# Kernel tuning notes

Measured on AMD Instinct MI355X. Metric: run time of the kernel, lower is better.

Reference implementation:

```python
import jax, jax.numpy as jnp
import numpy as np

N_FFT = 2048
HOP = 512


def _hann(n):
    # scipy.signal.get_window('hann', n, fftbins=True)
    return (0.5 - 0.5 * np.cos(2.0 * np.pi * np.arange(n) / n)).astype(np.float32)


def setup_inputs() -> dict:
    key = jax.random.key(0)
    k1, k2 = jax.random.split(key)
    B, T, F = 8, 1000, N_FFT // 2 + 1
    real_stft = jax.random.normal(k1, (B, 1, T, F), dtype=jnp.float32)
    imag_stft = jax.random.normal(k2, (B, 1, T, F), dtype=jnp.float32)

    # Windowed IDFT matrices, exactly as ISTFT.__init__ builds conv weights.
    n = N_FFT
    x, y = np.meshgrid(np.arange(n), np.arange(n))
    ang = 2.0 * np.pi * ((x * y) % n) / n  # angle of omega**(x*y), omega = exp(2*pi*i/n)
    win = _hann(n)  # win_length == n_fft -> pad_center is a no-op
    W_real = (np.cos(ang) / n * win[:, None]).astype(np.float32)
    W_imag = (np.sin(ang) / n * win[:, None]).astype(np.float32)

    return {
        "real_stft": real_stft,
        "imag_stft": imag_stft,
        "W_real": jnp.asarray(W_real),
        "W_imag": jnp.asarray(W_imag),
        "window": jnp.asarray(win),
        "length": 511488,  # HOP * (n_frames - 1) with n_frames = 1000
    }


def reference(real_stft, imag_stft, W_real, W_imag, window, length):
    n_fft, hop = N_FFT, HOP
    B = real_stft.shape[0]

    fr = jnp.swapaxes(real_stft[:, 0], 1, 2)  # (B, n_fft//2+1, T)
    fi = jnp.swapaxes(imag_stft[:, 0], 1, 2)
    # Hermitian symmetry -> full (B, n_fft, T) spectrum
    full_r = jnp.concatenate([fr, jnp.flip(fr[:, 1:-1, :], axis=1)], axis=1)
    full_i = jnp.concatenate([fi, -jnp.flip(fi[:, 1:-1, :], axis=1)], axis=1)

    # center=True and length given (static Python int)
    padded_length = length + n_fft
    n_frames = min(fr.shape[2], -(-padded_length // hop))

    # windowed real IFFT per frame: s[b, o, t]
    s = (jnp.einsum('oi,bit->bot', W_real, full_r[:, :, :n_frames])
         - jnp.einsum('oi,bit->bot', W_imag, full_i[:, :, :n_frames]))

    L = n_fft + hop * (n_frames - 1)
    # fused overlap-add via scatter-add
    idx = (jnp.arange(n_frames)[:, None] * hop + jnp.arange(n_fft)[None, :]).reshape(-1)
    frames = jnp.swapaxes(s, 1, 2).reshape(B, -1)  # (B, n_frames*n_fft)
    y = jnp.zeros((B, L), s.dtype).at[:, idx].add(frames)

    # window sum-square normalization (librosa.filters.window_sumsquare)
    wss = jnp.zeros((L,), window.dtype).at[idx].add(jnp.tile(window ** 2, n_frames))
    tiny = jnp.finfo(window.dtype).tiny
    nz = wss > tiny
    y = jnp.where(nz[None, :], y / jnp.where(nz, wss, 1.0)[None, :], y)

    start = n_fft // 2
    return y[:, start:start + length]
```

## Files before the change

### kernel.cpp

```cpp
#include <hip/hip_runtime.h>


#define N_FFT    2048
#define HOP      512
#define T_FRAMES 1000
#define F_BINS   1025
#define OUT_LEN  511488
#define FPB      8
#define BPB      125
#define OAF      5632

#define P(a) ((a) + ((a) >> 4))

__device__ __forceinline__ void cmul(float ar, float ai, float br, float bi,
                                     float& cr, float& ci) {
    cr = ar * br - ai * bi;
    ci = ar * bi + ai * br;
}

__global__ __launch_bounds__(256) void istft_oa_kernel(const float* __restrict__ re,
                                                       const float* __restrict__ im,
                                                       const float* __restrict__ win,
                                                       float* __restrict__ scratch,
                                                       float* __restrict__ out) {
    __shared__ __align__(16) float2 buf[1088];
    __shared__ __align__(16) float2 oa2[OAF / 2];

    const int j   = blockIdx.x;
    const int b   = blockIdx.y;
    const int tid = threadIdx.x;
    const int t0  = j * FPB;

    {
        float4* z4 = (float4*)oa2;
        #pragma unroll
        for (int e = 0; e < 6; ++e) {
            int idx = tid + 256 * e;
            if (idx < 1408) z4[idx] = make_float4(0.f, 0.f, 0.f, 0.f);
        }
    }

    const float Sc = 0.5f / 1024.f;
    const float2* w2v = (const float2*)win;

    for (int d = 0; d < FPB; ++d) {
        const int f = b * T_FRAMES + t0 + d;
        const float* fr = re + (size_t)f * F_BINS;
        const float* fi = im + (size_t)f * F_BINS;

        #pragma unroll
        for (int k0 = 0; k0 < 1024; k0 += 256) {
            int k = k0 + tid;
            float ar = fr[k];
            float ai = (k == 0) ? 0.f : fi[k];
            int mk = 1024 - k;
            float br = fr[mk];
            float bi = (mk == 1024) ? 0.f : fi[mk];
            float dr = ar - br, di = ai + bi;
            float ang = 3.14159265358979f * (float)k / 1024.f;
            float sn, cs;
            __sincosf(ang, &sn, &cs);
            float Zr = (ar + br - (cs * di + sn * dr)) * Sc;
            float Zi = (ai - bi + (cs * dr - sn * di)) * Sc;
            unsigned r10 = __brev((unsigned)k) >> 22;
            int rk = (int)(((r10 & 0x155u) << 1) | ((r10 >> 1) & 0x155u));
            buf[P(rk)] = make_float2(Zr, Zi);
        }
        __syncthreads();

        {
            int base = tid << 2;
            int i0 = P(base), i1 = P(base + 1), i2 = P(base + 2), i3 = P(base + 3);
            float2 a = buf[i0], bb = buf[i1], c = buf[i2], dd = buf[i3];
            float t0r = a.x + c.x,  t0i = a.y + c.y;
            float t1r = a.x - c.x,  t1i = a.y - c.y;
            float t2r = bb.x + dd.x, t2i = bb.y + dd.y;
            float t3r = bb.x - dd.x, t3i = bb.y - dd.y;
            buf[i0] = make_float2(t0r + t2r, t0i + t2i);
            buf[i1] = make_float2(t1r - t3i, t1i + t3r);
            buf[i2] = make_float2(t0r - t2r, t0i - t2i);
            buf[i3] = make_float2(t1r + t3i, t1i - t3r);
        }

        #pragma unroll
        for (int s = 1; s < 4; ++s) {
            __builtin_amdgcn_wave_barrier();
            const int hm = 1 << (2 * s);
            const int jj   = tid & (hm - 1);
            const int base = ((tid - jj) << 2) + jj;
            float ang = 1.57079632679f * (float)jj / (float)hm;
            float s1, c1;
            __sincosf(ang, &s1, &c1);
            float c2, s2, c3, s3;
            cmul(c1, s1, c1, s1, c2, s2);
            cmul(c2, s2, c1, s1, c3, s3);

            int i0 = P(base), i1 = P(base + hm), i2 = P(base + 2 * hm), i3 = P(base + 3 * hm);
            float2 a = buf[i0], bb = buf[i1], c = buf[i2], dd = buf[i3];
            float br_, bi_, cr_, ci_, dr_, di_;
            cmul(bb.x, bb.y, c1, s1, br_, bi_);
            cmul(c.x,  c.y,  c2, s2, cr_, ci_);
            cmul(dd.x, dd.y, c3, s3, dr_, di_);

            float t0r = a.x + cr_, t0i = a.y + ci_;
            float t1r = a.x - cr_, t1i = a.y - ci_;
            float t2r = br_ + dr_, t2i = bi_ + di_;
            float t3r = br_ - dr_, t3i = bi_ - di_;
            buf[i0] = make_float2(t0r + t2r, t0i + t2i);
            buf[i1] = make_float2(t1r - t3i, t1i + t3r);
            buf[i2] = make_float2(t0r - t2r, t0i - t2i);
            buf[i3] = make_float2(t1r + t3i, t1i - t3r);
        }
        __syncthreads();

        {
            float ang = 1.57079632679f * (float)tid / 256.f;
            float s1, c1;
            __sincosf(ang, &s1, &c1);
            float c2, s2, c3, s3;
            cmul(c1, s1, c1, s1, c2, s2);
            cmul(c2, s2, c1, s1, c3, s3);

            int i0 = P(tid), i1 = P(tid + 256), i2 = P(tid + 512), i3 = P(tid + 768);
            float2 a = buf[i0], bb = buf[i1], c = buf[i2], dd = buf[i3];
            float br_, bi_, cr_, ci_, dr_, di_;
            cmul(bb.x, bb.y, c1, s1, br_, bi_);
            cmul(c.x,  c.y,  c2, s2, cr_, ci_);
            cmul(dd.x, dd.y, c3, s3, dr_, di_);

            float t0r = a.x + cr_, t0i = a.y + ci_;
            float t1r = a.x - cr_, t1i = a.y - ci_;
            float t2r = br_ + dr_, t2i = bi_ + di_;
            float t3r = br_ - dr_, t3i = bi_ - di_;

            float2 z0 = make_float2(t0r + t2r, t0i + t2i);
            float2 z1 = make_float2(t1r - t3i, t1i + t3r);
            float2 z2 = make_float2(t0r - t2r, t0i - t2i);
            float2 z3 = make_float2(t1r + t3i, t1i - t3r);

            float2 w0 = w2v[tid],       w1 = w2v[tid + 256];
            float2 w2 = w2v[tid + 512], w3 = w2v[tid + 768];

            const int base2 = 256 * d;
            float2 v;
            v = oa2[base2 + tid];
            v.x += z0.x * w0.x;  v.y += z0.y * w0.y;
            oa2[base2 + tid] = v;
            v = oa2[base2 + tid + 256];
            v.x += z1.x * w1.x;  v.y += z1.y * w1.y;
            oa2[base2 + tid + 256] = v;
            v = oa2[base2 + tid + 512];
            v.x += z2.x * w2.x;  v.y += z2.y * w2.y;
            oa2[base2 + tid + 512] = v;
            v = oa2[base2 + tid + 768];
            v.x += z3.x * w3.x;  v.y += z3.y * w3.y;
            oa2[base2 + tid + 768] = v;
        }
        __syncthreads();
    }

    const float inv = 2.f / 3.f;
    const float4* oa4 = (const float4*)oa2;
    float4* o4 = (float4*)(out + (size_t)b * OUT_LEN + (size_t)4096 * j + 512);
    #pragma unroll
    for (int e = 0; e < 3; ++e) {
        int idx = tid + 256 * e;
        if (idx < 640) {
            float4 v = oa4[384 + idx];
            o4[idx] = make_float4(v.x * inv, v.y * inv, v.z * inv, v.w * inv);
        }
    }
    float4* sc4 = (float4*)(scratch + (((size_t)b * BPB + j) * 2) * 1536);
    #pragma unroll
    for (int e = 0; e < 3; ++e) {
        int idx = tid + 256 * e;
        float4 v = (idx < 384) ? oa4[idx] : oa4[640 + idx];
        sc4[idx] = v;
    }
}

__global__ __launch_bounds__(256) void seam_kernel(const float* __restrict__ scratch,
                                                   const float* __restrict__ win,
                                                   float* __restrict__ out) {
    const int g = blockIdx.x;
    const int b = blockIdx.y;

    #pragma unroll
    for (int e = 0; e < 6; ++e) {
        int i = threadIdx.x + 256 * e;
        int n = 4096 * g + i;
        int m = n - 1024;
        if (m < 0 || m >= OUT_LEN) continue;
        float s = 0.f;
        if (g > 0)
            s += scratch[(((size_t)b * BPB + (g - 1)) * 2 + 1) * 1536 + i];
        if (g < BPB)
            s += scratch[(((size_t)b * BPB + g) * 2) * 1536 + i];
        float r;
        if (n >= 1536 && n < 512000) {
            r = s * (2.f / 3.f);
        } else {
            int thi = n >> 9; if (thi > T_FRAMES - 1) thi = T_FRAMES - 1;
            int tlo = (n - (N_FFT - HOP)) >> 9; if (tlo < 0) tlo = 0;
            float wss = 0.f;
            for (int t = tlo; t <= thi; ++t) {
                float w = win[n - (t << 9)];
                wss += w * w;
            }
            r = (wss > 1.17549435e-38f) ? s / wss : s;
        }
        out[(size_t)b * OUT_LEN + m] = r;
    }
}

extern "C" void kernel_launch(void* const* d_in, const int* in_sizes, int n_in,
                              void* d_out, int out_size, void* d_ws, size_t ws_size,
                              hipStream_t stream) {
    const float* re  = (const float*)d_in[0];
    const float* im  = (const float*)d_in[1];
    const float* win = (const float*)d_in[4];
    float* out = (float*)d_out;

    float* scratch = (float*)d_ws;

    istft_oa_kernel<<<dim3(BPB, 8), 256, 0, stream>>>(re, im, win, scratch, out);
    seam_kernel<<<dim3(BPB + 1, 8), 256, 0, stream>>>(scratch, win, out);
}
```

Before: 148.7 us.

## Halve frames per block, hoist FFT twiddles into registers, set occupancy hint

Each block now processes 4 frames instead of 8, doubling the grid to 250 blocks per batch. The overlap-add buffer, output tiling and seam indexing are resized to match. Twiddle and pre-rotation sincos values are computed once per thread before the frame loop rather than recomputed for every frame. A min-blocks-per-CU launch bound is added, which adds parallelism and reduces transcendental work. The cost is more seam overhead, since the scratch traffic and the seam kernel's share of the output double, and more register pressure from the hoisted twiddles.

```diff
diff --git a/kernel.cpp b/kernel.cpp
--- a/kernel.cpp
+++ b/kernel.cpp
@@ -6,9 +6,9 @@
 #define T_FRAMES 1000
 #define F_BINS   1025
 #define OUT_LEN  511488
-#define FPB      8
-#define BPB      125
-#define OAF      5632
+#define FPB      4
+#define BPB      250
+#define OAF      3584
 
 #define P(a) ((a) + ((a) >> 4))
 
@@ -18,11 +18,11 @@
     ci = ar * bi + ai * br;
 }
 
-__global__ __launch_bounds__(256) void istft_oa_kernel(const float* __restrict__ re,
-                                                       const float* __restrict__ im,
-                                                       const float* __restrict__ win,
-                                                       float* __restrict__ scratch,
-                                                       float* __restrict__ out) {
+__global__ __launch_bounds__(256, 4) void istft_oa_kernel(const float* __restrict__ re,
+                                                          const float* __restrict__ im,
+                                                          const float* __restrict__ win,
+                                                          float* __restrict__ scratch,
+                                                          float* __restrict__ out) {
     __shared__ __align__(16) float2 buf[1088];
     __shared__ __align__(16) float2 oa2[OAF / 2];
 
@@ -34,10 +34,33 @@
     {
         float4* z4 = (float4*)oa2;
         #pragma unroll
-        for (int e = 0; e < 6; ++e) {
+        for (int e = 0; e < 4; ++e) {
             int idx = tid + 256 * e;
-            if (idx < 1408) z4[idx] = make_float4(0.f, 0.f, 0.f, 0.f);
-        }
+            if (idx < 896) z4[idx] = make_float4(0.f, 0.f, 0.f, 0.f);
+        }
+    }
+
+    float pcs[4], psn[4];
+    #pragma unroll
+    for (int q = 0; q < 4; ++q) {
+        float ang = 3.14159265358979f * (float)(tid + 256 * q) / 1024.f;
+        __sincosf(ang, &psn[q], &pcs[q]);
+    }
+    float tc1[4], ts1[4], tc2[4], ts2[4], tc3[4], ts3[4];
+    #pragma unroll
+    for (int s = 1; s < 4; ++s) {
+        const int hm = 1 << (2 * s);
+        const int jj = tid & (hm - 1);
+        float ang = 1.57079632679f * (float)jj / (float)hm;
+        __sincosf(ang, &ts1[s - 1], &tc1[s - 1]);
+        cmul(tc1[s-1], ts1[s-1], tc1[s-1], ts1[s-1], tc2[s-1], ts2[s-1]);
+        cmul(tc2[s-1], ts2[s-1], tc1[s-1], ts1[s-1], tc3[s-1], ts3[s-1]);
+    }
+    {
+        float ang = 1.57079632679f * (float)tid / 256.f;
+        __sincosf(ang, &ts1[3], &tc1[3]);
+        cmul(tc1[3], ts1[3], tc1[3], ts1[3], tc2[3], ts2[3]);
+        cmul(tc2[3], ts2[3], tc1[3], ts1[3], tc3[3], ts3[3]);
     }
 
     const float Sc = 0.5f / 1024.f;
@@ -49,17 +72,15 @@
         const float* fi = im + (size_t)f * F_BINS;
 
         #pragma unroll
-        for (int k0 = 0; k0 < 1024; k0 += 256) {
-            int k = k0 + tid;
+        for (int q = 0; q < 4; ++q) {
+            int k = 256 * q + tid;
             float ar = fr[k];
             float ai = (k == 0) ? 0.f : fi[k];
             int mk = 1024 - k;
             float br = fr[mk];
             float bi = (mk == 1024) ? 0.f : fi[mk];
             float dr = ar - br, di = ai + bi;
-            float ang = 3.14159265358979f * (float)k / 1024.f;
-            float sn, cs;
-            __sincosf(ang, &sn, &cs);
+            float cs = pcs[q], sn = psn[q];
             float Zr = (ar + br - (cs * di + sn * dr)) * Sc;
             float Zi = (ai - bi + (cs * dr - sn * di)) * Sc;
             unsigned r10 = __brev((unsigned)k) >> 22;
@@ -88,19 +109,16 @@
             const int hm = 1 << (2 * s);
             const int jj   = tid & (hm - 1);
             const int base = ((tid - jj) << 2) + jj;
-            float ang = 1.57079632679f * (float)jj / (float)hm;
-            float s1, c1;
-            __sincosf(ang, &s1, &c1);
-            float c2, s2, c3, s3;
-            cmul(c1, s1, c1, s1, c2, s2);
-            cmul(c2, s2, c1, s1, c3, s3);
+            const float c1 = tc1[s-1], s1v = ts1[s-1];
+            const float c2 = tc2[s-1], s2v = ts2[s-1];
+            const float c3 = tc3[s-1], s3v = ts3[s-1];
 
             int i0 = P(base), i1 = P(base + hm), i2 = P(base + 2 * hm), i3 = P(base + 3 * hm);
             float2 a = buf[i0], bb = buf[i1], c = buf[i2], dd = buf[i3];
             float br_, bi_, cr_, ci_, dr_, di_;
-            cmul(bb.x, bb.y, c1, s1, br_, bi_);
-            cmul(c.x,  c.y,  c2, s2, cr_, ci_);
-            cmul(dd.x, dd.y, c3, s3, dr_, di_);
+            cmul(bb.x, bb.y, c1, s1v, br_, bi_);
+            cmul(c.x,  c.y,  c2, s2v, cr_, ci_);
+            cmul(dd.x, dd.y, c3, s3v, dr_, di_);
 
             float t0r = a.x + cr_, t0i = a.y + ci_;
             float t1r = a.x - cr_, t1i = a.y - ci_;
@@ -114,19 +132,16 @@
         __syncthreads();
 
         {
-            float ang = 1.57079632679f * (float)tid / 256.f;
-            float s1, c1;
-            __sincosf(ang, &s1, &c1);
-            float c2, s2, c3, s3;
-            cmul(c1, s1, c1, s1, c2, s2);
-            cmul(c2, s2, c1, s1, c3, s3);
+            const float c1 = tc1[3], s1v = ts1[3];
+            const float c2 = tc2[3], s2v = ts2[3];
+            const float c3 = tc3[3], s3v = ts3[3];
 
             int i0 = P(tid), i1 = P(tid + 256), i2 = P(tid + 512), i3 = P(tid + 768);
             float2 a = buf[i0], bb = buf[i1], c = buf[i2], dd = buf[i3];
             float br_, bi_, cr_, ci_, dr_, di_;
-            cmul(bb.x, bb.y, c1, s1, br_, bi_);
-            cmul(c.x,  c.y,  c2, s2, cr_, ci_);
-            cmul(dd.x, dd.y, c3, s3, dr_, di_);
+            cmul(bb.x, bb.y, c1, s1v, br_, bi_);
+            cmul(c.x,  c.y,  c2, s2v, cr_, ci_);
+            cmul(dd.x, dd.y, c3, s3v, dr_, di_);
 
             float t0r = a.x + cr_, t0i = a.y + ci_;
             float t1r = a.x - cr_, t1i = a.y - ci_;
@@ -161,20 +176,16 @@
 
     const float inv = 2.f / 3.f;
     const float4* oa4 = (const float4*)oa2;
-    float4* o4 = (float4*)(out + (size_t)b * OUT_LEN + (size_t)4096 * j + 512);
+    if (tid < 128) {
+        float4 v = oa4[384 + tid];
+        float4* o4 = (float4*)(out + (size_t)b * OUT_LEN + (size_t)2048 * j + 512);
+        o4[tid] = make_float4(v.x * inv, v.y * inv, v.z * inv, v.w * inv);
+    }
+    float4* sc4 = (float4*)(scratch + (((size_t)b * BPB + j) * 2) * 1536);
     #pragma unroll
     for (int e = 0; e < 3; ++e) {
         int idx = tid + 256 * e;
-        if (idx < 640) {
-            float4 v = oa4[384 + idx];
-            o4[idx] = make_float4(v.x * inv, v.y * inv, v.z * inv, v.w * inv);
-        }
-    }
-    float4* sc4 = (float4*)(scratch + (((size_t)b * BPB + j) * 2) * 1536);
-    #pragma unroll
-    for (int e = 0; e < 3; ++e) {
-        int idx = tid + 256 * e;
-        float4 v = (idx < 384) ? oa4[idx] : oa4[640 + idx];
+        float4 v = (idx < 384) ? oa4[idx] : oa4[idx + 128];
         sc4[idx] = v;
     }
 }
@@ -188,7 +199,7 @@
     #pragma unroll
     for (int e = 0; e < 6; ++e) {
         int i = threadIdx.x + 256 * e;
-        int n = 4096 * g + i;
+        int n = 2048 * g + i;
         int m = n - 1024;
         if (m < 0 || m >= OUT_LEN) continue;
         float s = 0.f;
```

New measurement: 145.1 us. 1.02x faster.
